# Performance work log

Hardware: AMD Instinct MI355X
Metric: run time of the kernel (lower is better)

Reference implementation:

```python
import jax, jax.numpy as jnp
import numpy as np

B, C, CI, H, W = 8, 256, 128, 64, 64
EPS = 1e-5

def conv1x1(x, w, b):
    # x: [B,C,H,W], w: [O,C], b: [O]
    return jnp.einsum('bchw,oc->bohw', x, w) + b[None, :, None, None]

def avgpool2(x):
    b, c, h, w = x.shape
    return x.reshape(b, c, h // 2, 2, w // 2, 2).mean(axis=(3, 5))

def setup_inputs() -> dict:
    key = jax.random.key(0)
    ks = jax.random.split(key, 16)
    s = lambda fan: 1.0 / np.sqrt(fan)
    inp = {
        'q': jax.random.normal(ks[0], (B, C, H, W), jnp.float32),
        'k': jax.random.normal(ks[1], (B, C, H, W), jnp.float32),
        'v': jax.random.normal(ks[2], (B, C, H, W), jnp.float32),
        'Wg':  jax.random.normal(ks[3], (CI, C), jnp.float32) * s(C),
        'bg':  jax.random.normal(ks[4], (CI,), jnp.float32) * s(C),
        'Wth': jax.random.normal(ks[5], (CI, C), jnp.float32) * s(C),
        'bth': jax.random.normal(ks[6], (CI,), jnp.float32) * s(C),
        'Wph': jax.random.normal(ks[7], (CI, C), jnp.float32) * s(C),
        'bph': jax.random.normal(ks[8], (CI,), jnp.float32) * s(C),
        'Ww':  jax.random.normal(ks[9], (C, CI), jnp.float32) * s(CI),
        'bw':  jax.random.normal(ks[10], (C,), jnp.float32) * s(CI),
        'gamma': jax.random.normal(ks[11], (C,), jnp.float32) * 0.1 + 1.0,
        'beta':  jax.random.normal(ks[12], (C,), jnp.float32) * 0.1,
        'mean':  jax.random.normal(ks[13], (C,), jnp.float32) * 0.1,
        'var':   jax.random.uniform(ks[14], (C,), jnp.float32, 0.5, 1.5),
    }
    return inp

def reference(q, k, v, Wg, bg, Wth, bth, Wph, bph, Ww, bw, gamma, beta, mean, var):
    b = q.shape[0]
    # g branch on v, phi branch on q: 1x1 conv then 2x2 avg-pool (sub_sample)
    g_x = avgpool2(conv1x1(v, Wg, bg)).reshape(b, CI, -1)            # [B,CI,M]
    g_x = g_x.transpose(0, 2, 1)                                      # [B,M,CI]
    theta_x = conv1x1(k, Wth, bth).reshape(b, CI, -1).transpose(0, 2, 1)  # [B,N,CI]
    phi_x = avgpool2(conv1x1(q, Wph, bph)).reshape(b, CI, -1)        # [B,CI,M]
    f = jnp.einsum('bnc,bcm->bnm', theta_x, phi_x)                   # [B,N,M]
    f_div_C = jax.nn.softmax(f, axis=-1)
    y = jnp.einsum('bnm,bmc->bnc', f_div_C, g_x)                     # [B,N,CI]
    y = y.transpose(0, 2, 1).reshape(b, CI, H, W)
    W_y = conv1x1(y, Ww, bw)
    # BatchNorm2d (inference form)
    W_y = (W_y - mean[None, :, None, None]) * (gamma[None, :, None, None]
            * jax.lax.rsqrt(var + EPS)[None, :, None, None]) + beta[None, :, None, None]
    return W_y + v
```

## Files before the change

kernel.cpp:

```cpp
#include <hip/hip_runtime.h>
#include <cstddef>

typedef unsigned short u16;
typedef unsigned int u32;
typedef __attribute__((ext_vector_type(8))) __bf16 bf16x8;
typedef __attribute__((ext_vector_type(4))) float f32x4;

constexpr int kB = 8, kC = 256, kCI = 128, kN = 4096, kM = 1024;
constexpr float kEPS = 1e-5f;

__device__ __forceinline__ u16 f2bf(float f) {
    u32 u = __float_as_uint(f);
    u32 r = (u + 0x7fffu + ((u >> 16) & 1u)) >> 16;
    return (u16)r;
}

__global__ __launch_bounds__(256) void prep_kernel(const float* __restrict__ Wth,
                                                   const float* __restrict__ Wph,
                                                   const float* __restrict__ Wg,
                                                   const float* __restrict__ Ww,
                                                   const float* __restrict__ bw,
                                                   const float* __restrict__ gamma,
                                                   const float* __restrict__ beta,
                                                   const float* __restrict__ mean,
                                                   const float* __restrict__ var,
                                                   u16* __restrict__ Wthb,
                                                   u16* __restrict__ Wphb,
                                                   u16* __restrict__ Wgb,
                                                   u16* __restrict__ Wwsb,
                                                   float* __restrict__ bb) {
    int idx = blockIdx.x * 256 + threadIdx.x;
    if (idx < 32768) {
        Wthb[idx] = f2bf(Wth[idx]);
    } else if (idx < 65536) {
        int j = idx - 32768; Wphb[j] = f2bf(Wph[j]);
    } else if (idx < 98304) {
        int j = idx - 65536; Wgb[j] = f2bf(Wg[j]);
    } else {
        int j = idx - 98304;
        int co = j >> 7;
        float sc = gamma[co] * rsqrtf(var[co] + kEPS);
        Wwsb[j] = f2bf(Ww[j] * sc);
        if ((j & 127) == 0) bb[co] = (bw[co] - mean[co]) * sc + beta[co];
    }
}

__global__ __launch_bounds__(256) void pool_kernel(const float* __restrict__ in,
                                                   float* __restrict__ out) {
    int idx = blockIdx.x * 256 + threadIdx.x;
    int m  = idx & (kM - 1);
    int bc = idx >> 10;
    int mh = m >> 5, mw = m & 31;
    const float* p = in + ((size_t)bc * 64 + 2 * mh) * 64 + 2 * mw;
    float2 a = *(const float2*)p;
    float2 b = *(const float2*)(p + 64);
    out[idx] = 0.25f * (a.x + a.y + b.x + b.y);
}

template <int CMAJOR>
__global__ __launch_bounds__(256) void convp_kernel(const float* __restrict__ x,
                                                    const u16* __restrict__ Wb,
                                                    const float* __restrict__ bias,
                                                    u16* __restrict__ out, int Mn) {
    __shared__ __align__(16) u16 w_lds[128 * 72];
    __shared__ __align__(16) u16 x_lds[64 * 64];
    int t = threadIdx.x, b = blockIdx.y, n0 = blockIdx.x * 64;
    int w = t >> 6, lane = t & 63, l15 = lane & 15, quad = lane >> 4;
    int xn = t & 63, cbb = (t >> 6) * 2;

    f32x4 acc[8];
#pragma unroll
    for (int i = 0; i < 8; i++) acc[i] = (f32x4){0.f, 0.f, 0.f, 0.f};

    for (int c0 = 0; c0 < kC; c0 += 64) {
        __syncthreads();
#pragma unroll
        for (int i = 0; i < 4; i++) {
            int u = t + 256 * i;
            int ci = u >> 3, blk = u & 7;
            *(uint4*)&w_lds[ci * 72 + blk * 8] =
                *(const uint4*)&Wb[ci * kC + c0 + blk * 8];
        }
#pragma unroll
        for (int cc = 0; cc < 2; cc++) {
            int cb = cbb + cc;
            float f[8];
#pragma unroll
            for (int j = 0; j < 8; j++)
                f[j] = x[(size_t)(b * kC + c0 + cb * 8 + j) * Mn + n0 + xn];
            uint4 pk;
            pk.x = (u32)f2bf(f[0]) | ((u32)f2bf(f[1]) << 16);
            pk.y = (u32)f2bf(f[2]) | ((u32)f2bf(f[3]) << 16);
            pk.z = (u32)f2bf(f[4]) | ((u32)f2bf(f[5]) << 16);
            pk.w = (u32)f2bf(f[6]) | ((u32)f2bf(f[7]) << 16);
            *(uint4*)&x_lds[xn * 64 + ((cb ^ (xn & 7)) * 8)] = pk;
        }
        __syncthreads();

#pragma unroll
        for (int ks = 0; ks < 2; ks++) {
            int px = w * 16 + l15;
            bf16x8 xf = *(const bf16x8*)&x_lds[px * 64 + (((ks * 4 + quad) ^ (px & 7)) * 8)];
#pragma unroll
            for (int ct = 0; ct < 8; ct++) {
                bf16x8 wf = *(const bf16x8*)&w_lds[(ct * 16 + l15) * 72 + ks * 32 + quad * 8];
                if (CMAJOR)
                    acc[ct] = __builtin_amdgcn_mfma_f32_16x16x32_bf16(xf, wf, acc[ct], 0, 0, 0);
                else
                    acc[ct] = __builtin_amdgcn_mfma_f32_16x16x32_bf16(wf, xf, acc[ct], 0, 0, 0);
            }
        }
    }

    if (CMAJOR == 0) {
        int px = n0 + w * 16 + l15;
#pragma unroll
        for (int ct = 0; ct < 8; ct++) {
            int ci0 = ct * 16 + quad * 4;
            uint2 pk;
            pk.x = (u32)f2bf(acc[ct][0] + bias[ci0 + 0]) |
                   ((u32)f2bf(acc[ct][1] + bias[ci0 + 1]) << 16);
            pk.y = (u32)f2bf(acc[ct][2] + bias[ci0 + 2]) |
                   ((u32)f2bf(acc[ct][3] + bias[ci0 + 3]) << 16);
            *(uint2*)&out[(size_t)(b * Mn + px) * kCI + ci0] = pk;
        }
    } else {
        int px = n0 + w * 16 + quad * 4;
#pragma unroll
        for (int ct = 0; ct < 8; ct++) {
            int ci = ct * 16 + l15;
            float bs = bias[ci];
            uint2 pk;
            pk.x = (u32)f2bf(acc[ct][0] + bs) | ((u32)f2bf(acc[ct][1] + bs) << 16);
            pk.y = (u32)f2bf(acc[ct][2] + bs) | ((u32)f2bf(acc[ct][3] + bs) << 16);
            *(uint2*)&out[(size_t)(b * kCI + ci) * Mn + px] = pk;
        }
    }
}

__global__ __launch_bounds__(256) void attn_kernel(const u16* __restrict__ theta,
                                                   const u16* __restrict__ phi,
                                                   const u16* __restrict__ g,
                                                   u16* __restrict__ y) {
    __shared__ __align__(16) u16 th_lds[64 * 136];
    __shared__ __align__(16) u16 ph_lds[64 * 136];
    __shared__ __align__(16) u16 g_lds[128 * 72];
    __shared__ __align__(16) u16 p_lds[4 * 16 * 72];

    int t = threadIdx.x, b = blockIdx.y, n0 = blockIdx.x * 64;
    int w = t >> 6, lane = t & 63, l15 = lane & 15, quad = lane >> 4;

    const u16* thg = theta + (size_t)(b * kN + n0) * kCI;
#pragma unroll
    for (int it = 0; it < 4; it++) {
        int idx = t + 256 * it;
        int row = idx >> 4, col = (idx & 15) * 8;
        *(uint4*)&th_lds[row * 136 + col] = *(const uint4*)&thg[(size_t)row * kCI + col];
    }

    f32x4 oacc[8];
#pragma unroll
    for (int i = 0; i < 8; i++) oacc[i] = (f32x4){0.f, 0.f, 0.f, 0.f};
    float mprev[4], lsum[4];
#pragma unroll
    for (int r = 0; r < 4; r++) { mprev[r] = -1e30f; lsum[r] = 0.f; }

    const u16* phB = phi + (size_t)b * kM * kCI;
    const u16* gB  = g   + (size_t)b * kCI * kM;

    for (int c0 = 0; c0 < kM; c0 += 64) {
        __syncthreads();
#pragma unroll
        for (int it = 0; it < 4; it++) {
            int idx = t + 256 * it;
            int row = idx >> 4, col = (idx & 15) * 8;
            *(uint4*)&ph_lds[row * 136 + col] =
                *(const uint4*)&phB[(size_t)(c0 + row) * kCI + col];
        }
#pragma unroll
        for (int it = 0; it < 4; it++) {
            int idx = t + 256 * it;
            int row = idx >> 3, col = (idx & 7) * 8;
            *(uint4*)&g_lds[row * 72 + col] =
                *(const uint4*)&gB[(size_t)row * kM + c0 + col];
        }
        __syncthreads();

        f32x4 sacc[4];
#pragma unroll
        for (int mt = 0; mt < 4; mt++) sacc[mt] = (f32x4){0.f, 0.f, 0.f, 0.f};
#pragma unroll
        for (int kk = 0; kk < 4; kk++) {
            bf16x8 a = *(const bf16x8*)&th_lds[(w * 16 + l15) * 136 + kk * 32 + quad * 8];
#pragma unroll
            for (int mt = 0; mt < 4; mt++) {
                bf16x8 bb = *(const bf16x8*)&ph_lds[(mt * 16 + l15) * 136 + kk * 32 + quad * 8];
                sacc[mt] = __builtin_amdgcn_mfma_f32_16x16x32_bf16(a, bb, sacc[mt], 0, 0, 0);
            }
        }

#pragma unroll
        for (int r = 0; r < 4; r++) {
            float mc = fmaxf(fmaxf(sacc[0][r], sacc[1][r]), fmaxf(sacc[2][r], sacc[3][r]));
            mc = fmaxf(mc, __shfl_xor(mc, 1, 64));
            mc = fmaxf(mc, __shfl_xor(mc, 2, 64));
            mc = fmaxf(mc, __shfl_xor(mc, 4, 64));
            mc = fmaxf(mc, __shfl_xor(mc, 8, 64));
            float mn = fmaxf(mprev[r], mc);
            float alpha = __expf(mprev[r] - mn);
            mprev[r] = mn;
            float rs = 0.f;
#pragma unroll
            for (int mt = 0; mt < 4; mt++) {
                float p = __expf(sacc[mt][r] - mn);
                sacc[mt][r] = p;
                rs += p;
            }
            rs += __shfl_xor(rs, 1, 64);
            rs += __shfl_xor(rs, 2, 64);
            rs += __shfl_xor(rs, 4, 64);
            rs += __shfl_xor(rs, 8, 64);
            lsum[r] = lsum[r] * alpha + rs;
#pragma unroll
            for (int ct = 0; ct < 8; ct++) oacc[ct][r] *= alpha;
#pragma unroll
            for (int mt = 0; mt < 4; mt++)
                p_lds[w * 1152 + (quad * 4 + r) * 72 + mt * 16 + l15] = f2bf(sacc[mt][r]);
        }
        __syncthreads();

#pragma unroll
        for (int kk = 0; kk < 2; kk++) {
            bf16x8 a = *(const bf16x8*)&p_lds[w * 1152 + l15 * 72 + kk * 32 + quad * 8];
#pragma unroll
            for (int ct = 0; ct < 8; ct++) {
                bf16x8 bb = *(const bf16x8*)&g_lds[(ct * 16 + l15) * 72 + kk * 32 + quad * 8];
                oacc[ct] = __builtin_amdgcn_mfma_f32_16x16x32_bf16(a, bb, oacc[ct], 0, 0, 0);
            }
        }
    }

#pragma unroll
    for (int r = 0; r < 4; r++) {
        float inv = 1.0f / lsum[r];
        int n = n0 + w * 16 + quad * 4 + r;
        u16* yr = y + (size_t)(b * kN + n) * kCI;
#pragma unroll
        for (int ct = 0; ct < 8; ct++) yr[ct * 16 + l15] = f2bf(oacc[ct][r] * inv);
    }
}

__global__ __launch_bounds__(256) void final_kernel(const u16* __restrict__ y,
                                                    const u16* __restrict__ Wws,
                                                    const float* __restrict__ bb,
                                                    const float* __restrict__ v,
                                                    float* __restrict__ out) {
    __shared__ __align__(16) u16 y_lds[64 * 136];
    int t = threadIdx.x, b = blockIdx.y, n0 = blockIdx.x * 64;
    int w = t >> 6, lane = t & 63, l15 = lane & 15, quad = lane >> 4;

#pragma unroll
    for (int i = 0; i < 4; i++) {
        int u = t + 256 * i;
        int row = u >> 4, blk = u & 15;
        *(uint4*)&y_lds[row * 136 + blk * 8] =
            *(const uint4*)&y[(size_t)(b * kN + n0 + row) * kCI + blk * 8];
    }
    __syncthreads();

    bf16x8 af[4];
#pragma unroll
    for (int ks = 0; ks < 4; ks++)
        af[ks] = *(const bf16x8*)&y_lds[(w * 16 + l15) * 136 + ks * 32 + quad * 8];

#pragma unroll
    for (int ct = 0; ct < 16; ct++) {
        f32x4 a = (f32x4){0.f, 0.f, 0.f, 0.f};
#pragma unroll
        for (int ks = 0; ks < 4; ks++) {
            bf16x8 bf = *(const bf16x8*)&Wws[(ct * 16 + l15) * kCI + ks * 32 + quad * 8];
            a = __builtin_amdgcn_mfma_f32_16x16x32_bf16(af[ks], bf, a, 0, 0, 0);
        }
        int co = ct * 16 + l15;
        float bbv = bb[co];
        size_t base = (size_t)(b * kC + co) * kN + n0 + w * 16 + quad * 4;
        float4 vv = *(const float4*)&v[base];
        float4 ov;
        ov.x = a[0] + bbv + vv.x;
        ov.y = a[1] + bbv + vv.y;
        ov.z = a[2] + bbv + vv.z;
        ov.w = a[3] + bbv + vv.w;
        *(float4*)&out[base] = ov;
    }
}

extern "C" void kernel_launch(void* const* d_in, const int* in_sizes, int n_in,
                              void* d_out, int out_size, void* d_ws, size_t ws_size,
                              hipStream_t stream) {
    (void)in_sizes; (void)n_in; (void)out_size; (void)ws_size;
    const float* q     = (const float*)d_in[0];
    const float* k     = (const float*)d_in[1];
    const float* v     = (const float*)d_in[2];
    const float* Wg    = (const float*)d_in[3];
    const float* bg    = (const float*)d_in[4];
    const float* Wth   = (const float*)d_in[5];
    const float* bth   = (const float*)d_in[6];
    const float* Wph   = (const float*)d_in[7];
    const float* bph   = (const float*)d_in[8];
    const float* Ww    = (const float*)d_in[9];
    const float* bw    = (const float*)d_in[10];
    const float* gamma = (const float*)d_in[11];
    const float* beta  = (const float*)d_in[12];
    const float* mean  = (const float*)d_in[13];
    const float* var   = (const float*)d_in[14];
    float* out = (float*)d_out;

    float* ws = (float*)d_ws;
    float* qp    = ws;
    float* vp    = ws + 2097152;
    u16*   theta = (u16*)(ws + 4194304);
    u16*   phi   = (u16*)(ws + 6291456);
    u16*   gbuf  = (u16*)(ws + 6815744);
    u16*   ybuf  = (u16*)(ws + 7340032);
    u16*   Wthb  = (u16*)(ws + 9437184);
    u16*   Wphb  = Wthb + 32768;
    u16*   Wgb   = Wphb + 32768;
    u16*   Wwsb  = Wgb + 32768;
    float* bbuf  = (float*)(Wwsb + 32768);

    prep_kernel<<<dim3(512), 256, 0, stream>>>(Wth, Wph, Wg, Ww, bw, gamma, beta,
                                               mean, var, Wthb, Wphb, Wgb, Wwsb, bbuf);
    pool_kernel<<<dim3(8192), 256, 0, stream>>>(q, qp);
    pool_kernel<<<dim3(8192), 256, 0, stream>>>(v, vp);
    convp_kernel<0><<<dim3(64, 8), 256, 0, stream>>>(k, Wthb, bth, theta, kN);
    convp_kernel<0><<<dim3(16, 8), 256, 0, stream>>>(qp, Wphb, bph, phi, kM);
    convp_kernel<1><<<dim3(16, 8), 256, 0, stream>>>(vp, Wgb, bg, gbuf, kM);
    attn_kernel<<<dim3(64, 8), 256, 0, stream>>>(theta, phi, gbuf, ybuf);
    final_kernel<<<dim3(64, 8), 256, 0, stream>>>(ybuf, Wwsb, bbuf, v, out);
}
```

Measured before the change: 270.5 us.

## Fuse avgpool into conv kernels and restructure attention with register-held theta

Removes the separate pool kernels by averaging 2x2 windows inside the q and v 1x1-conv loads, which drops two launches and the fp32 pooled intermediates. The attention kernel is reworked: 128 threads per block, each wave owning 32 query rows whose theta fragments stay in registers. The score MMA is transposed so the softmax reductions need only two cross-lane shuffles, and the output rescale is skipped when the running max is unchanged. The P and g tiles get new LDS layouts. This raises register pressure and halves the waves per block, which may hurt occupancy and latency hiding.

Measured after the change: 270.8 us. About the same (+0.1%).

```diff
diff --git a/kernel.cpp b/kernel.cpp
--- a/kernel.cpp
+++ b/kernel.cpp
@@ -45,19 +45,7 @@
     }
 }
 
-__global__ __launch_bounds__(256) void pool_kernel(const float* __restrict__ in,
-                                                   float* __restrict__ out) {
-    int idx = blockIdx.x * 256 + threadIdx.x;
-    int m  = idx & (kM - 1);
-    int bc = idx >> 10;
-    int mh = m >> 5, mw = m & 31;
-    const float* p = in + ((size_t)bc * 64 + 2 * mh) * 64 + 2 * mw;
-    float2 a = *(const float2*)p;
-    float2 b = *(const float2*)(p + 64);
-    out[idx] = 0.25f * (a.x + a.y + b.x + b.y);
-}
-
-template <int CMAJOR>
+template <int CMAJOR, int POOL>
 __global__ __launch_bounds__(256) void convp_kernel(const float* __restrict__ x,
                                                     const u16* __restrict__ Wb,
                                                     const float* __restrict__ bias,
@@ -85,9 +73,21 @@
         for (int cc = 0; cc < 2; cc++) {
             int cb = cbb + cc;
             float f[8];
-#pragma unroll
-            for (int j = 0; j < 8; j++)
-                f[j] = x[(size_t)(b * kC + c0 + cb * 8 + j) * Mn + n0 + xn];
+            if (POOL) {
+                int p = n0 + xn, ph_ = p >> 5, pw_ = p & 31;
+#pragma unroll
+                for (int j = 0; j < 8; j++) {
+                    const float* src = x + ((size_t)(b * kC + c0 + cb * 8 + j) * 64
+                                            + 2 * ph_) * 64 + 2 * pw_;
+                    float2 a = *(const float2*)src;
+                    float2 b2 = *(const float2*)(src + 64);
+                    f[j] = 0.25f * (a.x + a.y + b2.x + b2.y);
+                }
+            } else {
+#pragma unroll
+                for (int j = 0; j < 8; j++)
+                    f[j] = x[(size_t)(b * kC + c0 + cb * 8 + j) * Mn + n0 + xn];
+            }
             uint4 pk;
             pk.x = (u32)f2bf(f[0]) | ((u32)f2bf(f[1]) << 16);
             pk.y = (u32)f2bf(f[2]) | ((u32)f2bf(f[3]) << 16);
@@ -138,115 +138,140 @@
     }
 }
 
-__global__ __launch_bounds__(256) void attn_kernel(const u16* __restrict__ theta,
+__global__ __launch_bounds__(128) void attn_kernel(const u16* __restrict__ theta,
                                                    const u16* __restrict__ phi,
                                                    const u16* __restrict__ g,
                                                    u16* __restrict__ y) {
-    __shared__ __align__(16) u16 th_lds[64 * 136];
-    __shared__ __align__(16) u16 ph_lds[64 * 136];
-    __shared__ __align__(16) u16 g_lds[128 * 72];
-    __shared__ __align__(16) u16 p_lds[4 * 16 * 72];
+    __shared__ __align__(16) u16 ph_lds[8192];
+    __shared__ __align__(16) u16 g_lds[8192];
+    __shared__ __align__(16) u16 p_lds[4096];
 
     int t = threadIdx.x, b = blockIdx.y, n0 = blockIdx.x * 64;
     int w = t >> 6, lane = t & 63, l15 = lane & 15, quad = lane >> 4;
 
-    const u16* thg = theta + (size_t)(b * kN + n0) * kCI;
-#pragma unroll
-    for (int it = 0; it < 4; it++) {
-        int idx = t + 256 * it;
-        int row = idx >> 4, col = (idx & 15) * 8;
-        *(uint4*)&th_lds[row * 136 + col] = *(const uint4*)&thg[(size_t)row * kCI + col];
-    }
-
-    f32x4 oacc[8];
-#pragma unroll
-    for (int i = 0; i < 8; i++) oacc[i] = (f32x4){0.f, 0.f, 0.f, 0.f};
-    float mprev[4], lsum[4];
-#pragma unroll
-    for (int r = 0; r < 4; r++) { mprev[r] = -1e30f; lsum[r] = 0.f; }
+    bf16x8 thf[2][4];
+    const u16* thB = theta + ((size_t)(b * kN) + n0 + w * 32) * kCI;
+#pragma unroll
+    for (int nt = 0; nt < 2; nt++)
+#pragma unroll
+        for (int ks = 0; ks < 4; ks++)
+            thf[nt][ks] = *(const bf16x8*)&thB[(size_t)(nt * 16 + l15) * kCI + ks * 32 + quad * 8];
+
+    f32x4 oacc[8][2];
+#pragma unroll
+    for (int ct = 0; ct < 8; ct++) {
+        oacc[ct][0] = (f32x4){0.f, 0.f, 0.f, 0.f};
+        oacc[ct][1] = (f32x4){0.f, 0.f, 0.f, 0.f};
+    }
+    float m_[2] = {-1e30f, -1e30f}, l_[2] = {0.f, 0.f};
 
     const u16* phB = phi + (size_t)b * kM * kCI;
     const u16* gB  = g   + (size_t)b * kCI * kM;
+    u16* pw = p_lds + w * 2048;
 
     for (int c0 = 0; c0 < kM; c0 += 64) {
         __syncthreads();
 #pragma unroll
-        for (int it = 0; it < 4; it++) {
-            int idx = t + 256 * it;
-            int row = idx >> 4, col = (idx & 15) * 8;
-            *(uint4*)&ph_lds[row * 136 + col] =
-                *(const uint4*)&phB[(size_t)(c0 + row) * kCI + col];
-        }
-#pragma unroll
-        for (int it = 0; it < 4; it++) {
-            int idx = t + 256 * it;
-            int row = idx >> 3, col = (idx & 7) * 8;
-            *(uint4*)&g_lds[row * 72 + col] =
-                *(const uint4*)&gB[(size_t)row * kM + c0 + col];
+        for (int it = 0; it < 8; it++) {
+            int u = t + 128 * it;
+            int row = u >> 4, cb = u & 15;
+            *(uint4*)&ph_lds[(cb >> 2) * 2048 + row * 32 + (cb & 3) * 8] =
+                *(const uint4*)&phB[(size_t)(c0 + row) * kCI + cb * 8];
+        }
+#pragma unroll
+        for (int it = 0; it < 8; it++) {
+            int u = t + 128 * it;
+            int ci = u >> 3, mb = u & 7;
+            *(uint4*)&g_lds[(mb >> 2) * 4096 + ci * 32 + (mb & 3) * 8] =
+                *(const uint4*)&gB[(size_t)ci * kM + c0 + mb * 8];
         }
         __syncthreads();
 
-        f32x4 sacc[4];
-#pragma unroll
-        for (int mt = 0; mt < 4; mt++) sacc[mt] = (f32x4){0.f, 0.f, 0.f, 0.f};
-#pragma unroll
-        for (int kk = 0; kk < 4; kk++) {
-            bf16x8 a = *(const bf16x8*)&th_lds[(w * 16 + l15) * 136 + kk * 32 + quad * 8];
+        f32x4 sacc[4][2];
+#pragma unroll
+        for (int mt = 0; mt < 4; mt++) {
+            sacc[mt][0] = (f32x4){0.f, 0.f, 0.f, 0.f};
+            sacc[mt][1] = (f32x4){0.f, 0.f, 0.f, 0.f};
+        }
+#pragma unroll
+        for (int ks = 0; ks < 4; ks++)
 #pragma unroll
             for (int mt = 0; mt < 4; mt++) {
-                bf16x8 bb = *(const bf16x8*)&ph_lds[(mt * 16 + l15) * 136 + kk * 32 + quad * 8];
-                sacc[mt] = __builtin_amdgcn_mfma_f32_16x16x32_bf16(a, bb, sacc[mt], 0, 0, 0);
-            }
-        }
-
-#pragma unroll
-        for (int r = 0; r < 4; r++) {
-            float mc = fmaxf(fmaxf(sacc[0][r], sacc[1][r]), fmaxf(sacc[2][r], sacc[3][r]));
-            mc = fmaxf(mc, __shfl_xor(mc, 1, 64));
-            mc = fmaxf(mc, __shfl_xor(mc, 2, 64));
-            mc = fmaxf(mc, __shfl_xor(mc, 4, 64));
-            mc = fmaxf(mc, __shfl_xor(mc, 8, 64));
-            float mn = fmaxf(mprev[r], mc);
-            float alpha = __expf(mprev[r] - mn);
-            mprev[r] = mn;
+                bf16x8 a = *(const bf16x8*)&ph_lds[ks * 2048 + (mt * 16 + l15) * 32 + quad * 8];
+                sacc[mt][0] = __builtin_amdgcn_mfma_f32_16x16x32_bf16(a, thf[0][ks], sacc[mt][0], 0, 0, 0);
+                sacc[mt][1] = __builtin_amdgcn_mfma_f32_16x16x32_bf16(a, thf[1][ks], sacc[mt][1], 0, 0, 0);
+            }
+
+#pragma unroll
+        for (int nt = 0; nt < 2; nt++) {
+            float mc = -1e30f;
+#pragma unroll
+            for (int mt = 0; mt < 4; mt++)
+#pragma unroll
+                for (int r = 0; r < 4; r++) mc = fmaxf(mc, sacc[mt][nt][r]);
+            mc = fmaxf(mc, __shfl_xor(mc, 16, 64));
+            mc = fmaxf(mc, __shfl_xor(mc, 32, 64));
+            float mp = m_[nt];
+            float mn = fmaxf(mp, mc);
+            int resc = __any(mn != mp);
+            float alpha = __expf(mp - mn);
+            m_[nt] = mn;
             float rs = 0.f;
 #pragma unroll
-            for (int mt = 0; mt < 4; mt++) {
-                float p = __expf(sacc[mt][r] - mn);
-                sacc[mt][r] = p;
-                rs += p;
-            }
-            rs += __shfl_xor(rs, 1, 64);
-            rs += __shfl_xor(rs, 2, 64);
-            rs += __shfl_xor(rs, 4, 64);
-            rs += __shfl_xor(rs, 8, 64);
-            lsum[r] = lsum[r] * alpha + rs;
-#pragma unroll
-            for (int ct = 0; ct < 8; ct++) oacc[ct][r] *= alpha;
-#pragma unroll
             for (int mt = 0; mt < 4; mt++)
-                p_lds[w * 1152 + (quad * 4 + r) * 72 + mt * 16 + l15] = f2bf(sacc[mt][r]);
-        }
-        __syncthreads();
-
-#pragma unroll
-        for (int kk = 0; kk < 2; kk++) {
-            bf16x8 a = *(const bf16x8*)&p_lds[w * 1152 + l15 * 72 + kk * 32 + quad * 8];
+#pragma unroll
+                for (int r = 0; r < 4; r++) {
+                    float p = __expf(sacc[mt][nt][r] - mn);
+                    sacc[mt][nt][r] = p;
+                    rs += p;
+                }
+            rs += __shfl_xor(rs, 16, 64);
+            rs += __shfl_xor(rs, 32, 64);
+            l_[nt] = l_[nt] * alpha + rs;
+            if (resc) {
+#pragma unroll
+                for (int ct = 0; ct < 8; ct++)
+#pragma unroll
+                    for (int r = 0; r < 4; r++) oacc[ct][nt][r] *= alpha;
+            }
+#pragma unroll
+            for (int mt = 0; mt < 4; mt++)
+#pragma unroll
+                for (int h = 0; h < 2; h++) {
+                    u32 ue = __float_as_uint(sacc[mt][nt][2 * h]) + 0x8000u;
+                    u32 uo = __float_as_uint(sacc[mt][nt][2 * h + 1]) + 0x8000u;
+                    u32 d = (ue >> 16) | (uo & 0xffff0000u);
+                    int m = mt * 16 + quad * 4 + 2 * h;
+                    int off = ((m >> 5) * 2 + nt) * 512 + (((m >> 3) & 3) * 16 + l15) * 8 + (m & 7);
+                    *(u32*)&pw[off] = d;
+                }
+        }
+
+#pragma unroll
+        for (int ks2 = 0; ks2 < 2; ks2++) {
+            bf16x8 b0 = *(const bf16x8*)&pw[(ks2 * 2 + 0) * 512 + (quad * 16 + l15) * 8];
+            bf16x8 b1 = *(const bf16x8*)&pw[(ks2 * 2 + 1) * 512 + (quad * 16 + l15) * 8];
 #pragma unroll
             for (int ct = 0; ct < 8; ct++) {
-                bf16x8 bb = *(const bf16x8*)&g_lds[(ct * 16 + l15) * 72 + kk * 32 + quad * 8];
-                oacc[ct] = __builtin_amdgcn_mfma_f32_16x16x32_bf16(a, bb, oacc[ct], 0, 0, 0);
-            }
-        }
-    }
-
-#pragma unroll
-    for (int r = 0; r < 4; r++) {
-        float inv = 1.0f / lsum[r];
-        int n = n0 + w * 16 + quad * 4 + r;
-        u16* yr = y + (size_t)(b * kN + n) * kCI;
-#pragma unroll
-        for (int ct = 0; ct < 8; ct++) yr[ct * 16 + l15] = f2bf(oacc[ct][r] * inv);
+                bf16x8 a = *(const bf16x8*)&g_lds[ks2 * 4096 + (ct * 16 + l15) * 32 + quad * 8];
+                oacc[ct][0] = __builtin_amdgcn_mfma_f32_16x16x32_bf16(a, b0, oacc[ct][0], 0, 0, 0);
+                oacc[ct][1] = __builtin_amdgcn_mfma_f32_16x16x32_bf16(a, b1, oacc[ct][1], 0, 0, 0);
+            }
+        }
+    }
+
+#pragma unroll
+    for (int nt = 0; nt < 2; nt++) {
+        float inv = 1.0f / l_[nt];
+        int n = n0 + w * 32 + nt * 16 + l15;
+        u16* yr = y + ((size_t)(b * kN) + n) * kCI + quad * 4;
+#pragma unroll
+        for (int ct = 0; ct < 8; ct++) {
+            uint2 pk;
+            pk.x = (u32)f2bf(oacc[ct][nt][0] * inv) | ((u32)f2bf(oacc[ct][nt][1] * inv) << 16);
+            pk.y = (u32)f2bf(oacc[ct][nt][2] * inv) | ((u32)f2bf(oacc[ct][nt][3] * inv) << 16);
+            *(uint2*)&yr[ct * 16] = pk;
+        }
     }
 }
 
@@ -315,14 +340,12 @@
     const float* var   = (const float*)d_in[14];
     float* out = (float*)d_out;
 
-    float* ws = (float*)d_ws;
-    float* qp    = ws;
-    float* vp    = ws + 2097152;
-    u16*   theta = (u16*)(ws + 4194304);
-    u16*   phi   = (u16*)(ws + 6291456);
-    u16*   gbuf  = (u16*)(ws + 6815744);
-    u16*   ybuf  = (u16*)(ws + 7340032);
-    u16*   Wthb  = (u16*)(ws + 9437184);
+    u16* wsu = (u16*)d_ws;
+    u16*   theta = wsu;
+    u16*   phi   = theta + 4194304;
+    u16*   gbuf  = phi + 1048576;
+    u16*   ybuf  = gbuf + 1048576;
+    u16*   Wthb  = ybuf + 4194304;
     u16*   Wphb  = Wthb + 32768;
     u16*   Wgb   = Wphb + 32768;
     u16*   Wwsb  = Wgb + 32768;
@@ -330,11 +353,9 @@
 
     prep_kernel<<<dim3(512), 256, 0, stream>>>(Wth, Wph, Wg, Ww, bw, gamma, beta,
                                                mean, var, Wthb, Wphb, Wgb, Wwsb, bbuf);
-    pool_kernel<<<dim3(8192), 256, 0, stream>>>(q, qp);
-    pool_kernel<<<dim3(8192), 256, 0, stream>>>(v, vp);
-    convp_kernel<0><<<dim3(64, 8), 256, 0, stream>>>(k, Wthb, bth, theta, kN);
-    convp_kernel<0><<<dim3(16, 8), 256, 0, stream>>>(qp, Wphb, bph, phi, kM);
-    convp_kernel<1><<<dim3(16, 8), 256, 0, stream>>>(vp, Wgb, bg, gbuf, kM);
-    attn_kernel<<<dim3(64, 8), 256, 0, stream>>>(theta, phi, gbuf, ybuf);
+    convp_kernel<0, 0><<<dim3(64, 8), 256, 0, stream>>>(k, Wthb, bth, theta, kN);
+    convp_kernel<0, 1><<<dim3(16, 8), 256, 0, stream>>>(q, Wphb, bph, phi, kM);
+    convp_kernel<1, 1><<<dim3(16, 8), 256, 0, stream>>>(v, Wgb, bg, gbuf, kM);
+    attn_kernel<<<dim3(64, 8), 128, 0, stream>>>(theta, phi, gbuf, ybuf);
     final_kernel<<<dim3(64, 8), 256, 0, stream>>>(ybuf, Wwsb, bbuf, v, out);
 }
```
